# Optimization experiments

Hardware: AMD Instinct MI355X
Metric: run time of the kernel (lower is better)

The kernel has to match this reference:

```python
import jax, jax.numpy as jnp
import numpy as np


def setup_inputs() -> dict:
    key = jax.random.key(0)
    k1, k2 = jax.random.split(key)
    B, C, H, W = 8, 128, 192, 256
    a = jax.random.normal(k1, (B, C, H, W), dtype=jnp.float32)
    b = jax.random.normal(k2, (B, C, H, W), dtype=jnp.float32)
    return {"a": a, "b": b, "max_displacement": 40}


def reference(a, b, max_displacement):
    """Horizontal correlation cost volume.

    out[:, ctr, h, w] = sum_c a[:, c, h, w] * b[:, c, h, w - (D - ctr)]
    for ctr in 0..D (out-of-range b treated as zero), matching the torch
    shift-and-pad loop over displacements i = -D..0.
    """
    D = max_displacement
    W = a.shape[-1]
    # Pad b once on the left by D; then the shifted slice for index ctr is
    # bp[..., ctr:ctr+W]  (static slices -> jit-friendly, no big stack kept).
    bp = jnp.pad(b, ((0, 0), (0, 0), (0, 0), (D, 0)))
    outs = [jnp.einsum('bchw,bchw->bhw', a, bp[..., ctr:ctr + W])
            for ctr in range(D + 1)]  # small fixed loop over D+1 displacements
    return jnp.stack(outs, axis=1)  # [B, D+1, H, W]
```

## Files before the change

### kernel.cpp

```cpp
#include <hip/hip_runtime.h>


constexpr int Bsz = 8, Cch = 128, Hh = 192, Ww = 256, NC = 41;
constexpr int CHW = Hh * Ww;
constexpr int LDB = 40;
constexpr int A_BYTES = 256 * LDB * 2;
constexpr int OSTRIDE = 260;

using short8  = __attribute__((ext_vector_type(8))) short;
using floatx4 = __attribute__((ext_vector_type(4))) float;

__device__ inline unsigned short f2bf(float x) {
    unsigned int u = __float_as_uint(x);
    u += 0x7fffu + ((u >> 16) & 1u);
    return (unsigned short)(u >> 16);
}

__global__ __launch_bounds__(256, 3)
void corr_mfma(const float* __restrict__ A, const float* __restrict__ B,
               float* __restrict__ O) {
    __shared__ __align__(16) unsigned char smem[44800];
    unsigned short* aT   = (unsigned short*)smem;
    unsigned short* bT   = (unsigned short*)(smem + A_BYTES);
    float*          outp = (float*)smem;

    const int tid  = threadIdx.x;
    const int lane = tid & 63, wave = tid >> 6;
    const int row  = blockIdx.x;
    const int bb   = row / Hh, h = row - bb * Hh;

    const float* base_a = A + (size_t)bb * Cch * CHW + (size_t)h * Ww;
    const float* base_b = B + (size_t)bb * Cch * CHW + (size_t)h * Ww;

    const int c8 = tid & 3;
    const int w4 = tid >> 2;
    const int wi = lane & 15, kg = lane >> 4;

    floatx4 acc[4][4];
#pragma unroll
    for (int i = 0; i < 4; ++i)
#pragma unroll
        for (int j = 0; j < 4; ++j) acc[i][j] = (floatx4)0.0f;

    for (int c0 = 0; c0 < Cch; c0 += 32) {
        __syncthreads();
        if (tid < 160) {
            int u = tid >> 2, cz = (tid & 3) * 8;
            *(short8*)(bT + u * LDB + cz) = (short8)0;
        }
        {
            float4 la[8];
#pragma unroll
            for (int i = 0; i < 8; ++i)
                la[i] = *(const float4*)(base_a + (size_t)(c0 + c8 * 8 + i) * CHW + w4 * 4);
            const float* laf = (const float*)la;
#pragma unroll
            for (int r = 0; r < 4; ++r) {
                short8 s;
#pragma unroll
                for (int i = 0; i < 8; ++i) s[i] = (short)f2bf(laf[i * 4 + r]);
                *(short8*)(aT + (w4 * 4 + r) * LDB + c8 * 8) = s;
            }
        }
        {
            float4 lb[8];
#pragma unroll
            for (int i = 0; i < 8; ++i)
                lb[i] = *(const float4*)(base_b + (size_t)(c0 + c8 * 8 + i) * CHW + w4 * 4);
            const float* lbf = (const float*)lb;
#pragma unroll
            for (int r = 0; r < 4; ++r) {
                short8 s;
#pragma unroll
                for (int i = 0; i < 8; ++i) s[i] = (short)f2bf(lbf[i * 4 + r]);
                *(short8*)(bT + (40 + w4 * 4 + r) * LDB + c8 * 8) = s;
            }
        }
        __syncthreads();

#pragma unroll
        for (int i = 0; i < 4; ++i) {
            const int w0 = wave * 64 + i * 16;
            short8 afrag_a = *(const short8*)(aT + (w0 + wi) * LDB + kg * 8);
#pragma unroll
            for (int j = 0; j < 4; ++j) {
                const int u0 = w0 + 16 * j;
                short8 bfrag_b = *(const short8*)(bT + (u0 + wi) * LDB + kg * 8);
                acc[i][j] = __builtin_amdgcn_mfma_f32_16x16x32_bf16(bfrag_b, afrag_a,
                                                                    acc[i][j], 0, 0, 0);
            }
        }
    }

    __syncthreads();
#pragma unroll
    for (int i = 0; i < 4; ++i) {
        const int w0 = wave * 64 + i * 16;
#pragma unroll
        for (int j = 0; j < 4; ++j) {
#pragma unroll
            for (int r = 0; r < 4; ++r) {
                int ctr = 16 * j + (kg * 4 + r) - wi;
                if ((unsigned)ctr <= 40u) outp[ctr * OSTRIDE + w0 + wi] = acc[i][j][r];
            }
        }
    }
    __syncthreads();
    float* obase = O + ((size_t)bb * NC * Hh + (size_t)h) * Ww;
    for (int idx = tid; idx < NC * 64; idx += 256) {
        int ctr = idx >> 6, q = idx & 63;
        float4 v = *(const float4*)(outp + ctr * OSTRIDE + q * 4);
        *(float4*)(obase + (size_t)ctr * CHW + q * 4) = v;
    }
}

extern "C" void kernel_launch(void* const* d_in, const int* in_sizes, int n_in,
                              void* d_out, int out_size, void* d_ws, size_t ws_size,
                              hipStream_t stream) {
    const float* a = (const float*)d_in[0];
    const float* b = (const float*)d_in[1];
    float* out = (float*)d_out;
    corr_mfma<<<dim3(Bsz * Hh), dim3(256), 0, stream>>>(a, b, out);
}
```

Before: 409.1 us.

## Double-buffer global loads in registers and widen blocks to 512 threads

The block grows to 512 threads (8 waves), each wave covering 32 output columns with a 2x4 MFMA tile. It reuses five shared b fragments across the two a rows. Global fp32 loads for the next channel chunk are issued into two register buffers while the current chunk is converted and consumed, with a fully unrolled four-step schedule. Plain syncthreads is replaced by explicit lgkmcnt waits and raw barriers. The aim is to hide global-load latency and raise occupancy, at the cost of more registers per thread and a hand-ordered schedule tied to C=128.

New measurement: 408.0 us. About the same (-0.3%).

```diff
diff --git a/kernel.cpp b/kernel.cpp
--- a/kernel.cpp
+++ b/kernel.cpp
@@ -7,8 +7,9 @@
 constexpr int A_BYTES = 256 * LDB * 2;
 constexpr int OSTRIDE = 260;
 
-using short8  = __attribute__((ext_vector_type(8))) short;
-using floatx4 = __attribute__((ext_vector_type(4))) float;
+using sh4 = __attribute__((ext_vector_type(4))) short;
+using sh8 = __attribute__((ext_vector_type(8))) short;
+using fx4 = __attribute__((ext_vector_type(4))) float;
 
 __device__ inline unsigned short f2bf(float x) {
     unsigned int u = __float_as_uint(x);
@@ -16,7 +17,7 @@
     return (unsigned short)(u >> 16);
 }
 
-__global__ __launch_bounds__(256, 3)
+__global__ __launch_bounds__(512, 4)
 void corr_mfma(const float* __restrict__ A, const float* __restrict__ B,
                float* __restrict__ O) {
     __shared__ __align__(16) unsigned char smem[44800];
@@ -32,82 +33,111 @@
     const float* base_a = A + (size_t)bb * Cch * CHW + (size_t)h * Ww;
     const float* base_b = B + (size_t)bb * Cch * CHW + (size_t)h * Ww;
 
-    const int c8 = tid & 3;
-    const int w4 = tid >> 2;
+    const int cg = tid & 7;
+    const int w4 = tid >> 3;
     const int wi = lane & 15, kg = lane >> 4;
 
-    floatx4 acc[4][4];
+    const float* pa0 = base_a + (size_t)(cg * 4) * CHW + w4 * 4;
+    const float* pb0 = base_b + (size_t)(cg * 4) * CHW + w4 * 4;
+
+    fx4 acc[2][4];
 #pragma unroll
-    for (int i = 0; i < 4; ++i)
+    for (int i = 0; i < 2; ++i)
 #pragma unroll
-        for (int j = 0; j < 4; ++j) acc[i][j] = (floatx4)0.0f;
+        for (int j = 0; j < 4; ++j) acc[i][j] = (fx4)0.0f;
 
-    for (int c0 = 0; c0 < Cch; c0 += 32) {
-        __syncthreads();
-        if (tid < 160) {
-            int u = tid >> 2, cz = (tid & 3) * 8;
-            *(short8*)(bT + u * LDB + cz) = (short8)0;
-        }
-        {
-            float4 la[8];
-#pragma unroll
-            for (int i = 0; i < 8; ++i)
-                la[i] = *(const float4*)(base_a + (size_t)(c0 + c8 * 8 + i) * CHW + w4 * 4);
-            const float* laf = (const float*)la;
-#pragma unroll
-            for (int r = 0; r < 4; ++r) {
-                short8 s;
-#pragma unroll
-                for (int i = 0; i < 8; ++i) s[i] = (short)f2bf(laf[i * 4 + r]);
-                *(short8*)(aT + (w4 * 4 + r) * LDB + c8 * 8) = s;
-            }
-        }
-        {
-            float4 lb[8];
-#pragma unroll
-            for (int i = 0; i < 8; ++i)
-                lb[i] = *(const float4*)(base_b + (size_t)(c0 + c8 * 8 + i) * CHW + w4 * 4);
-            const float* lbf = (const float*)lb;
-#pragma unroll
-            for (int r = 0; r < 4; ++r) {
-                short8 s;
-#pragma unroll
-                for (int i = 0; i < 8; ++i) s[i] = (short)f2bf(lbf[i * 4 + r]);
-                *(short8*)(bT + (40 + w4 * 4 + r) * LDB + c8 * 8) = s;
-            }
-        }
-        __syncthreads();
+    float4 rA[2][4], rB[2][4];
 
-#pragma unroll
-        for (int i = 0; i < 4; ++i) {
-            const int w0 = wave * 64 + i * 16;
-            short8 afrag_a = *(const short8*)(aT + (w0 + wi) * LDB + kg * 8);
-#pragma unroll
-            for (int j = 0; j < 4; ++j) {
-                const int u0 = w0 + 16 * j;
-                short8 bfrag_b = *(const short8*)(bT + (u0 + wi) * LDB + kg * 8);
-                acc[i][j] = __builtin_amdgcn_mfma_f32_16x16x32_bf16(bfrag_b, afrag_a,
-                                                                    acc[i][j], 0, 0, 0);
-            }
-        }
+#define ISSUE(S, K)                                                           \
+    _Pragma("unroll")                                                         \
+    for (int i = 0; i < 4; ++i)                                               \
+        rA[S][i] = *(const float4*)(pa0 + (size_t)((K) * 32 + i) * CHW);      \
+    _Pragma("unroll")                                                         \
+    for (int i = 0; i < 4; ++i)                                               \
+        rB[S][i] = *(const float4*)(pb0 + (size_t)((K) * 32 + i) * CHW);
+
+#define CONV_STORE(S)                                                         \
+    {                                                                         \
+        const float* fa = (const float*)&rA[S][0];                            \
+        const float* fb = (const float*)&rB[S][0];                            \
+        _Pragma("unroll")                                                     \
+        for (int r = 0; r < 4; ++r) {                                         \
+            sh4 s;                                                            \
+            _Pragma("unroll")                                                 \
+            for (int i = 0; i < 4; ++i) s[i] = (short)f2bf(fa[i * 4 + r]);    \
+            *(sh4*)(aT + (w4 * 4 + r) * LDB + cg * 4) = s;                    \
+        }                                                                     \
+        _Pragma("unroll")                                                     \
+        for (int r = 0; r < 4; ++r) {                                         \
+            sh4 s;                                                            \
+            _Pragma("unroll")                                                 \
+            for (int i = 0; i < 4; ++i) s[i] = (short)f2bf(fb[i * 4 + r]);    \
+            *(sh4*)(bT + (40 + w4 * 4 + r) * LDB + cg * 4) = s;               \
+        }                                                                     \
     }
 
-    __syncthreads();
+#define MFMA_STEP()                                                           \
+    {                                                                         \
+        const int w0 = wave * 32;                                             \
+        sh8 afr[2], bfr[5];                                                   \
+        _Pragma("unroll")                                                     \
+        for (int i = 0; i < 2; ++i)                                           \
+            afr[i] = *(const sh8*)(aT + (w0 + i * 16 + wi) * LDB + kg * 8);   \
+        _Pragma("unroll")                                                     \
+        for (int t = 0; t < 5; ++t)                                           \
+            bfr[t] = *(const sh8*)(bT + (w0 + t * 16 + wi) * LDB + kg * 8);   \
+        _Pragma("unroll")                                                     \
+        for (int i = 0; i < 2; ++i)                                           \
+            _Pragma("unroll")                                                 \
+            for (int j = 0; j < 4; ++j)                                       \
+                acc[i][j] = __builtin_amdgcn_mfma_f32_16x16x32_bf16(          \
+                    bfr[i + j], afr[i], acc[i][j], 0, 0, 0);                  \
+    }
+
+#define DS_BAR()                                           \
+    asm volatile("s_waitcnt lgkmcnt(0)" ::: "memory");     \
+    __builtin_amdgcn_s_barrier();                          \
+    asm volatile("" ::: "memory");
+
+    ISSUE(0, 0)
+    if (tid < 320) {
+        int u = tid >> 3, cz = (tid & 7) * 4;
+        *(sh4*)(bT + u * LDB + cz) = (sh4)0;
+    }
+    ISSUE(1, 1)
+    CONV_STORE(0)
+    ISSUE(0, 2)
+    DS_BAR()
+    MFMA_STEP()
+    DS_BAR()
+    CONV_STORE(1)
+    ISSUE(1, 3)
+    DS_BAR()
+    MFMA_STEP()
+    DS_BAR()
+    CONV_STORE(0)
+    DS_BAR()
+    MFMA_STEP()
+    DS_BAR()
+    CONV_STORE(1)
+    DS_BAR()
+    MFMA_STEP()
+
+    DS_BAR()
 #pragma unroll
-    for (int i = 0; i < 4; ++i) {
-        const int w0 = wave * 64 + i * 16;
+    for (int i = 0; i < 2; ++i) {
+        const int w0 = wave * 32 + i * 16;
 #pragma unroll
-        for (int j = 0; j < 4; ++j) {
+        for (int j = 0; j < 4; ++j)
 #pragma unroll
             for (int r = 0; r < 4; ++r) {
                 int ctr = 16 * j + (kg * 4 + r) - wi;
                 if ((unsigned)ctr <= 40u) outp[ctr * OSTRIDE + w0 + wi] = acc[i][j][r];
             }
-        }
     }
-    __syncthreads();
+    DS_BAR()
     float* obase = O + ((size_t)bb * NC * Hh + (size_t)h) * Ww;
-    for (int idx = tid; idx < NC * 64; idx += 256) {
+    for (int idx = tid; idx < NC * 64; idx += 512) {
         int ctr = idx >> 6, q = idx & 63;
         float4 v = *(const float4*)(outp + ctr * OSTRIDE + q * 4);
         *(float4*)(obase + (size_t)ctr * CHW + q * 4) = v;
@@ -120,5 +150,5 @@
     const float* a = (const float*)d_in[0];
     const float* b = (const float*)d_in[1];
     float* out = (float*)d_out;
-    corr_mfma<<<dim3(Bsz * Hh), dim3(256), 0, stream>>>(a, b, out);
+    corr_mfma<<<dim3(Bsz * Hh), dim3(512), 0, stream>>>(a, b, out);
 }
```
